# Optimization experiments

Measured on AMD Instinct MI355X. Metric: run time of the kernel, lower is better.

## Reference

```python
import jax, jax.numpy as jnp
import numpy as np

DIM = 2048
N_HEADS = 32
N_KV_HEADS = 8
HEAD_DIM = DIM // N_HEADS  # 64
GROUP = N_HEADS // N_KV_HEADS  # 4
ROPE_BASE = 10000.0


def setup_inputs() -> dict:
    key = jax.random.key(0)
    k1, k2, k3, k4, k5 = jax.random.split(key, 5)
    b, s = 1, 2048
    scale = 1.0 / np.sqrt(DIM)
    return {
        "x": jax.random.normal(k1, (b, s, DIM), dtype=jnp.float32),
        # weights stored as (in, out); equivalent math to torch Linear (x @ W.T)
        "wq": jax.random.normal(k2, (DIM, N_HEADS * HEAD_DIM), dtype=jnp.float32) * scale,
        "wk": jax.random.normal(k3, (DIM, N_KV_HEADS * HEAD_DIM), dtype=jnp.float32) * scale,
        "wv": jax.random.normal(k4, (DIM, N_KV_HEADS * HEAD_DIM), dtype=jnp.float32) * scale,
        "wo": jax.random.normal(k5, (N_HEADS * HEAD_DIM, DIM), dtype=jnp.float32) * scale,
    }


def _rope_cos_sin(seq_len, dtype):
    inv_freq = 1.0 / (ROPE_BASE ** (jnp.arange(0, HEAD_DIM, 2, dtype=jnp.float32) / HEAD_DIM))
    t = jnp.arange(seq_len, dtype=jnp.float32)
    freqs = jnp.outer(t, inv_freq)              # [s, hd/2]
    emb = jnp.concatenate([freqs, freqs], -1)   # [s, hd]
    return jnp.cos(emb).astype(dtype), jnp.sin(emb).astype(dtype)


def _rotate_half(x):
    x1, x2 = x[..., : HEAD_DIM // 2], x[..., HEAD_DIM // 2 :]
    return jnp.concatenate([-x2, x1], axis=-1)


def reference(x, wq, wk, wv, wo):
    b, s, _ = x.shape
    q = (x @ wq).reshape(b, s, N_HEADS, HEAD_DIM)
    k = (x @ wk).reshape(b, s, N_KV_HEADS, HEAD_DIM)
    v = (x @ wv).reshape(b, s, N_KV_HEADS, HEAD_DIM)

    cos, sin = _rope_cos_sin(s, x.dtype)
    cos = cos[None, :, None, :]  # [1, s, 1, hd] broadcast over batch & heads
    sin = sin[None, :, None, :]
    q = q * cos + _rotate_half(q) * sin
    k = k * cos + _rotate_half(k) * sin

    # GQA: repeat KV heads (repeat_interleave along head dim)
    k = jnp.repeat(k, GROUP, axis=2)  # [b, s, n_heads, hd]
    v = jnp.repeat(v, GROUP, axis=2)

    q = q.transpose(0, 2, 1, 3)  # [b, h, s, d]
    k = k.transpose(0, 2, 1, 3)
    v = v.transpose(0, 2, 1, 3)

    scores = jnp.einsum("bhqd,bhkd->bhqk", q, k) / jnp.sqrt(jnp.asarray(HEAD_DIM, x.dtype))
    attn = jax.nn.softmax(scores, axis=-1)
    out = jnp.einsum("bhqk,bhkd->bhqd", attn, v)
    out = out.transpose(0, 2, 1, 3).reshape(b, s, N_HEADS * HEAD_DIM)
    return out @ wo
```

## Files before the change

kernel.cpp:

```cpp
#include <hip/hip_runtime.h>
#include <hip/hip_bf16.h>

typedef __bf16 bf16x8 __attribute__((ext_vector_type(8)));
typedef __bf16 bf16x4 __attribute__((ext_vector_type(4)));
typedef __bf16 bf16x2 __attribute__((ext_vector_type(2)));
typedef float fx4 __attribute__((ext_vector_type(4)));
typedef float fx16 __attribute__((ext_vector_type(16)));

#define AS1 __attribute__((address_space(1)))
#define AS3 __attribute__((address_space(3)))

__global__ __launch_bounds__(256) void prep(const float4* __restrict__ X, __bf16* __restrict__ Xb,
                                            const float* __restrict__ wq, const float* __restrict__ wk,
                                            const float* __restrict__ wv, const float* __restrict__ wo,
                                            __bf16* __restrict__ WqkvT, __bf16* __restrict__ WoT) {
    const int bx = blockIdx.x;
    if (bx < 4096) {
        const int i = bx * 256 + threadIdx.x;
        const float4 v = X[i];
        bf16x4 o = { (__bf16)v.x, (__bf16)v.y, (__bf16)v.z, (__bf16)v.w };
        *(bf16x4*)(Xb + (size_t)i * 4) = o;
        return;
    }
    constexpr int K = 2048;
    __shared__ float t[64][33];
    const int tt = bx - 4096;
    const float* W; __bf16* Wt; int N, loc;
    if (tt < 2048)      { W = wq; Wt = WqkvT;                       N = 2048; loc = tt; }
    else if (tt < 2560) { W = wk; Wt = WqkvT + (size_t)2048 * 2048; N = 512;  loc = tt - 2048; }
    else if (tt < 3072) { W = wv; Wt = WqkvT + (size_t)2560 * 2048; N = 512;  loc = tt - 2560; }
    else                { W = wo; Wt = WoT;                         N = 2048; loc = tt - 3072; }
    const int k0 = (loc & 31) * 64, n0 = (loc >> 5) * 32;
    const int tx = threadIdx.x & 31, ty = threadIdx.x >> 5;
#pragma unroll
    for (int i = 0; i < 8; ++i)
        t[ty + i * 8][tx] = W[(size_t)(k0 + ty + i * 8) * N + n0 + tx];
    __syncthreads();
#pragma unroll
    for (int i = 0; i < 4; ++i) {
        const int nn = ty + i * 8;
        bf16x2 o = { (__bf16)t[tx * 2][nn], (__bf16)t[tx * 2 + 1][nn] };
        *(bf16x2*)&Wt[(size_t)(n0 + nn) * K + k0 + tx * 2] = o;
    }
}

__global__ __launch_bounds__(256) void gemm_qkv(const __bf16* __restrict__ A, const __bf16* __restrict__ Bt,
                                                __bf16* __restrict__ Qr, __bf16* __restrict__ Kr,
                                                __bf16* __restrict__ Vt) {
    constexpr int K = 2048;
    constexpr int BUF = 192 * 32;
    __shared__ __align__(16) __bf16 sm[4][BUF];
    const int tid = threadIdx.x;
    const int wave = tid >> 6, lane = tid & 63;
    const int quad = lane >> 4, l16 = lane & 15;
    const int m0 = blockIdx.x * 128, n0 = blockIdx.y * 64;
    fx4 acc[2][4] = {};

    const int r4 = lane >> 2;
    const int c8s = ((lane & 3) ^ ((r4 >> 1) & 3)) * 8;
    const __bf16* csrc[3]; int cdst[3];
#pragma unroll
    for (int it = 0; it < 3; ++it) {
        const int idx = wave * 3 + it;
        if (idx < 8) {
            csrc[it] = A + (size_t)(m0 + idx * 16 + r4) * K + c8s;
            cdst[it] = idx * 512 + lane * 8;
        } else {
            const int s = idx - 8;
            csrc[it] = Bt + (size_t)(n0 + s * 16 + r4) * K + c8s;
            cdst[it] = 4096 + s * 512 + lane * 8;
        }
    }
    const int colr = (quad ^ ((l16 >> 1) & 3)) * 8;
    const int arow = (wave * 32 + l16) * 32 + colr;
    const int brow = 4096 + l16 * 32 + colr;

    auto compute = [&](const __bf16* cb) {
        bf16x8 af[2], bfr[4];
#pragma unroll
        for (int i = 0; i < 2; ++i) af[i] = *(const bf16x8*)&cb[arow + i * 512];
#pragma unroll
        for (int j = 0; j < 4; ++j) bfr[j] = *(const bf16x8*)&cb[brow + j * 512];
#pragma unroll
        for (int i = 0; i < 2; ++i)
#pragma unroll
            for (int j = 0; j < 4; ++j)
                acc[i][j] = __builtin_amdgcn_mfma_f32_16x16x32_bf16(af[i], bfr[j], acc[i][j], 0, 0, 0);
    };

#pragma unroll
    for (int pt = 0; pt < 3; ++pt)
#pragma unroll
        for (int it = 0; it < 3; ++it)
            __builtin_amdgcn_global_load_lds((const AS1 void*)(csrc[it] + pt * 32),
                                             (AS3 void*)&sm[pt][cdst[it]], 16, 0, 0);

#pragma unroll 1
    for (int t = 0; t < 61; ++t) {
        asm volatile("s_waitcnt vmcnt(6) lgkmcnt(0)" ::: "memory");
        __builtin_amdgcn_s_barrier();
        const int kofs = (t + 3) * 32;
#pragma unroll
        for (int it = 0; it < 3; ++it)
            __builtin_amdgcn_global_load_lds((const AS1 void*)(csrc[it] + kofs),
                                             (AS3 void*)&sm[(t + 3) & 3][cdst[it]], 16, 0, 0);
        compute(sm[t & 3]);
    }
    asm volatile("s_waitcnt vmcnt(6) lgkmcnt(0)" ::: "memory"); __builtin_amdgcn_s_barrier(); compute(sm[1]);
    asm volatile("s_waitcnt vmcnt(3) lgkmcnt(0)" ::: "memory"); __builtin_amdgcn_s_barrier(); compute(sm[2]);
    asm volatile("s_waitcnt vmcnt(0) lgkmcnt(0)" ::: "memory"); __builtin_amdgcn_s_barrier(); compute(sm[3]);

    const int by = blockIdx.y;
    if (by < 40) {
        const float scale = (by < 32) ? 0.18033688011112042f : 1.0f;
        __bf16* base = (by < 32) ? (Qr + (size_t)by * 2048 * 64)
                                 : (Kr + (size_t)(by - 32) * 2048 * 64);
#pragma unroll
        for (int jj = 0; jj < 2; ++jj) {
            const int dlo = jj * 16 + l16;
            const float inv = __builtin_amdgcn_exp2f(-(float)dlo * 0.41524101186092029f);
#pragma unroll
            for (int i = 0; i < 2; ++i)
#pragma unroll
                for (int r = 0; r < 4; ++r) {
                    const int s = m0 + wave * 32 + i * 16 + quad * 4 + r;
                    float sn, cs;
                    __sincosf((float)s * inv, &sn, &cs);
                    const float lo = acc[i][jj][r], hv = acc[i][jj + 2][r];
                    base[(size_t)s * 64 + dlo]      = (__bf16)((lo * cs - hv * sn) * scale);
                    base[(size_t)s * 64 + dlo + 32] = (__bf16)((hv * cs + lo * sn) * scale);
                }
        }
    } else {
        __bf16* vb = Vt + (size_t)(by - 40) * 64 * 2048;
#pragma unroll
        for (int i = 0; i < 2; ++i)
#pragma unroll
            for (int j = 0; j < 4; ++j) {
                const int d = j * 16 + l16;
                const int s0 = m0 + wave * 32 + i * 16 + quad * 4;
                bf16x4 p;
#pragma unroll
                for (int r = 0; r < 4; ++r) p[r] = (__bf16)acc[i][j][r];
                *(bf16x4*)&vb[(size_t)d * 2048 + s0] = p;
            }
    }
}

__global__ __launch_bounds__(256) void gemm_out(const __bf16* __restrict__ A, const __bf16* __restrict__ Bt,
                                                float* __restrict__ C) {
    constexpr int K = 2048;
    constexpr int BUF = 192 * 32;
    __shared__ __align__(16) __bf16 sm[4][BUF];
    const int tid = threadIdx.x;
    const int wave = tid >> 6, lane = tid & 63;
    const int quad = lane >> 4, l16 = lane & 15;
    const int m0 = blockIdx.x * 128, n0 = blockIdx.y * 64;
    fx4 acc[2][4] = {};

    const int r4 = lane >> 2;
    const int c8s = ((lane & 3) ^ ((r4 >> 1) & 3)) * 8;
    const __bf16* csrc[3]; int cdst[3];
#pragma unroll
    for (int it = 0; it < 3; ++it) {
        const int idx = wave * 3 + it;
        if (idx < 8) {
            csrc[it] = A + (size_t)(m0 + idx * 16 + r4) * K + c8s;
            cdst[it] = idx * 512 + lane * 8;
        } else {
            const int s = idx - 8;
            csrc[it] = Bt + (size_t)(n0 + s * 16 + r4) * K + c8s;
            cdst[it] = 4096 + s * 512 + lane * 8;
        }
    }
    const int colr = (quad ^ ((l16 >> 1) & 3)) * 8;
    const int arow = (wave * 32 + l16) * 32 + colr;
    const int brow = 4096 + l16 * 32 + colr;

    auto compute = [&](const __bf16* cb) {
        bf16x8 af[2], bfr[4];
#pragma unroll
        for (int i = 0; i < 2; ++i) af[i] = *(const bf16x8*)&cb[arow + i * 512];
#pragma unroll
        for (int j = 0; j < 4; ++j) bfr[j] = *(const bf16x8*)&cb[brow + j * 512];
#pragma unroll
        for (int i = 0; i < 2; ++i)
#pragma unroll
            for (int j = 0; j < 4; ++j)
                acc[i][j] = __builtin_amdgcn_mfma_f32_16x16x32_bf16(af[i], bfr[j], acc[i][j], 0, 0, 0);
    };

#pragma unroll
    for (int pt = 0; pt < 3; ++pt)
#pragma unroll
        for (int it = 0; it < 3; ++it)
            __builtin_amdgcn_global_load_lds((const AS1 void*)(csrc[it] + pt * 32),
                                             (AS3 void*)&sm[pt][cdst[it]], 16, 0, 0);

#pragma unroll 1
    for (int t = 0; t < 61; ++t) {
        asm volatile("s_waitcnt vmcnt(6) lgkmcnt(0)" ::: "memory");
        __builtin_amdgcn_s_barrier();
        const int kofs = (t + 3) * 32;
#pragma unroll
        for (int it = 0; it < 3; ++it)
            __builtin_amdgcn_global_load_lds((const AS1 void*)(csrc[it] + kofs),
                                             (AS3 void*)&sm[(t + 3) & 3][cdst[it]], 16, 0, 0);
        compute(sm[t & 3]);
    }
    asm volatile("s_waitcnt vmcnt(6) lgkmcnt(0)" ::: "memory"); __builtin_amdgcn_s_barrier(); compute(sm[1]);
    asm volatile("s_waitcnt vmcnt(3) lgkmcnt(0)" ::: "memory"); __builtin_amdgcn_s_barrier(); compute(sm[2]);
    asm volatile("s_waitcnt vmcnt(0) lgkmcnt(0)" ::: "memory"); __builtin_amdgcn_s_barrier(); compute(sm[3]);

#pragma unroll
    for (int i = 0; i < 2; ++i)
#pragma unroll
        for (int j = 0; j < 4; ++j) {
            const int row = m0 + wave * 32 + i * 16 + quad * 4;
            const int col = n0 + j * 16 + l16;
#pragma unroll
            for (int r = 0; r < 4; ++r)
                C[(size_t)(row + r) * 2048 + col] = acc[i][j][r];
        }
}

__global__ __launch_bounds__(512, 4) void flash_attn(const __bf16* __restrict__ Qr, const __bf16* __restrict__ Kr,
                                                     const __bf16* __restrict__ Vt, __bf16* __restrict__ O) {
    constexpr int S = 2048;
    __shared__ __align__(16) __bf16 smem[2][4 * 64 * 72];
    const int qt = blockIdx.x, h = blockIdx.y, kvh = h >> 2;
    const int tid = threadIdx.x, wave = tid >> 6, lane = tid & 63;
    const int grp = wave >> 2, w4 = wave & 3;
    const int l32 = lane & 31, hi = lane >> 5;
    const int goff = grp * 2 * 4608;

    const int qrow = qt * 128 + w4 * 32 + l32;
    const __bf16* qptr = Qr + ((size_t)h * S + qrow) * 64;
    bf16x8 qf[4];
#pragma unroll
    for (int kc = 0; kc < 4; ++kc) qf[kc] = *(const bf16x8*)(qptr + kc * 16 + hi * 8);

    const __bf16* Kbase = Kr + (size_t)kvh * S * 64;
    const __bf16* Vbase = Vt + (size_t)kvh * 64 * S;

    const int gtid = tid & 255;
    const int krow = gtid >> 3;
    const int kcol = (gtid & 7) * 8;
    const int vslot = (kcol & 48) | ((kcol & 8) >> 1);

    bf16x8 kreg0 = *(const bf16x8*)(Kbase + (size_t)(grp * 64 + krow) * 64 + kcol);
    bf16x8 kreg1 = *(const bf16x8*)(Kbase + (size_t)(grp * 64 + 32 + krow) * 64 + kcol);
    bf16x8 vreg0 = *(const bf16x8*)(Vbase + (size_t)krow * S + grp * 64 + kcol);
    bf16x8 vreg1 = *(const bf16x8*)(Vbase + (size_t)(32 + krow) * S + grp * 64 + kcol);

    fx16 ov0, ov1;
#pragma unroll
    for (int i = 0; i < 16; ++i) { ov0[i] = 0.f; ov1[i] = 0.f; }
    float l_acc = 0.f;

    {
        __bf16* nK = &smem[0][goff];
        __bf16* nV = nK + 4608;
        *(bf16x8*)&nK[krow * 72 + kcol] = kreg0;
        *(bf16x8*)&nK[(32 + krow) * 72 + kcol] = kreg1;
        bf16x4 v0lo = { vreg0[0], vreg0[1], vreg0[2], vreg0[3] };
        bf16x4 v0hi = { vreg0[4], vreg0[5], vreg0[6], vreg0[7] };
        bf16x4 v1lo = { vreg1[0], vreg1[1], vreg1[2], vreg1[3] };
        bf16x4 v1hi = { vreg1[4], vreg1[5], vreg1[6], vreg1[7] };
        *(bf16x4*)&nV[krow * 72 + vslot]            = v0lo;
        *(bf16x4*)&nV[krow * 72 + vslot + 8]        = v0hi;
        *(bf16x4*)&nV[(32 + krow) * 72 + vslot]     = v1lo;
        *(bf16x4*)&nV[(32 + krow) * 72 + vslot + 8] = v1hi;
        const int kt1 = 2 + grp;
        kreg0 = *(const bf16x8*)(Kbase + (size_t)(kt1 * 64 + krow) * 64 + kcol);
        kreg1 = *(const bf16x8*)(Kbase + (size_t)(kt1 * 64 + 32 + krow) * 64 + kcol);
        vreg0 = *(const bf16x8*)(Vbase + (size_t)krow * S + kt1 * 64 + kcol);
        vreg1 = *(const bf16x8*)(Vbase + (size_t)(32 + krow) * S + kt1 * 64 + kcol);
    }
    __syncthreads();

    for (int it = 0; it < 16; ++it) {
        __bf16* lKg = &smem[it & 1][goff];
        __bf16* lVg = lKg + 4608;

        if (it + 1 < 16) {
            __bf16* nK = &smem[(it + 1) & 1][goff];
            __bf16* nV = nK + 4608;
            *(bf16x8*)&nK[krow * 72 + kcol] = kreg0;
            *(bf16x8*)&nK[(32 + krow) * 72 + kcol] = kreg1;
            bf16x4 v0lo = { vreg0[0], vreg0[1], vreg0[2], vreg0[3] };
            bf16x4 v0hi = { vreg0[4], vreg0[5], vreg0[6], vreg0[7] };
            bf16x4 v1lo = { vreg1[0], vreg1[1], vreg1[2], vreg1[3] };
            bf16x4 v1hi = { vreg1[4], vreg1[5], vreg1[6], vreg1[7] };
            *(bf16x4*)&nV[krow * 72 + vslot]            = v0lo;
            *(bf16x4*)&nV[krow * 72 + vslot + 8]        = v0hi;
            *(bf16x4*)&nV[(32 + krow) * 72 + vslot]     = v1lo;
            *(bf16x4*)&nV[(32 + krow) * 72 + vslot + 8] = v1hi;
            const int it2 = (it + 2 < 16) ? it + 2 : 15;
            const int ktn = it2 * 2 + grp;
            kreg0 = *(const bf16x8*)(Kbase + (size_t)(ktn * 64 + krow) * 64 + kcol);
            kreg1 = *(const bf16x8*)(Kbase + (size_t)(ktn * 64 + 32 + krow) * 64 + kcol);
            vreg0 = *(const bf16x8*)(Vbase + (size_t)krow * S + ktn * 64 + kcol);
            vreg1 = *(const bf16x8*)(Vbase + (size_t)(32 + krow) * S + ktn * 64 + kcol);
        }

        fx16 sc0, sc1;
#pragma unroll
        for (int i = 0; i < 16; ++i) { sc0[i] = 0.f; sc1[i] = 0.f; }
#pragma unroll
        for (int kc = 0; kc < 4; ++kc) {
            const bf16x8 a0 = *(const bf16x8*)&lKg[l32 * 72 + kc * 16 + hi * 8];
            const bf16x8 a1 = *(const bf16x8*)&lKg[(32 + l32) * 72 + kc * 16 + hi * 8];
            sc0 = __builtin_amdgcn_mfma_f32_32x32x16_bf16(a0, qf[kc], sc0, 0, 0, 0);
            sc1 = __builtin_amdgcn_mfma_f32_32x32x16_bf16(a1, qf[kc], sc1, 0, 0, 0);
        }

#pragma unroll
        for (int h2 = 0; h2 < 2; ++h2) {
#pragma unroll
            for (int c = 0; c < 2; ++c) {
                bf16x8 pb;
#pragma unroll
                for (int j = 0; j < 8; ++j) {
                    const float sv = h2 ? sc1[c * 8 + j] : sc0[c * 8 + j];
                    const float p = __builtin_amdgcn_exp2f(sv);
                    l_acc += p;
                    pb[j] = (__bf16)p;
                }
                const int kcv = h2 * 2 + c;
                const bf16x8 va0 = *(const bf16x8*)&lVg[l32 * 72 + kcv * 16 + hi * 8];
                const bf16x8 va1 = *(const bf16x8*)&lVg[(32 + l32) * 72 + kcv * 16 + hi * 8];
                ov0 = __builtin_amdgcn_mfma_f32_32x32x16_bf16(va0, pb, ov0, 0, 0, 0);
                ov1 = __builtin_amdgcn_mfma_f32_32x32x16_bf16(va1, pb, ov1, 0, 0, 0);
            }
        }
        __syncthreads();
    }

    const float l_pair = l_acc + __shfl_xor(l_acc, 32, 64);

    fx4* lO = (fx4*)&smem[0][0];
    float* lL = (float*)(&smem[0][0] + 16384);
    if (grp == 1) {
#pragma unroll
        for (int ic = 0; ic < 4; ++ic) {
            fx4 c0, c1;
#pragma unroll
            for (int r = 0; r < 4; ++r) { c0[r] = ov0[ic * 4 + r]; c1[r] = ov1[ic * 4 + r]; }
            lO[(ic * 4 + w4) * 64 + lane] = c0;
            lO[((ic + 4) * 4 + w4) * 64 + lane] = c1;
        }
        if (hi == 0) lL[w4 * 32 + l32] = l_pair;
    }
    __syncthreads();
    if (grp == 0) {
#pragma unroll
        for (int ic = 0; ic < 4; ++ic) {
            const fx4 c0 = lO[(ic * 4 + w4) * 64 + lane];
            const fx4 c1 = lO[((ic + 4) * 4 + w4) * 64 + lane];
#pragma unroll
            for (int r = 0; r < 4; ++r) { ov0[ic * 4 + r] += c0[r]; ov1[ic * 4 + r] += c1[r]; }
        }
        const float inv_l = 1.0f / (l_pair + lL[w4 * 32 + l32]);
#pragma unroll
        for (int dt = 0; dt < 2; ++dt)
#pragma unroll
            for (int rg2 = 0; rg2 < 4; ++rg2) {
                bf16x4 o4;
#pragma unroll
                for (int r = 0; r < 4; ++r)
                    o4[r] = (__bf16)((dt ? ov1[rg2 * 4 + r] : ov0[rg2 * 4 + r]) * inv_l);
                const int col = h * 64 + dt * 32 + rg2 * 8 + hi * 4;
                *(bf16x4*)(O + (size_t)qrow * 2048 + col) = o4;
            }
    }
}

extern "C" void kernel_launch(void* const* d_in, const int* in_sizes, int n_in,
                              void* d_out, int out_size, void* d_ws, size_t ws_size,
                              hipStream_t stream) {
    const float* x  = (const float*)d_in[0];
    const float* wq = (const float*)d_in[1];
    const float* wk = (const float*)d_in[2];
    const float* wv = (const float*)d_in[3];
    const float* wo = (const float*)d_in[4];
    float* out = (float*)d_out;
    char* ws = (char*)d_ws;

    __bf16* Xb    = (__bf16*)ws;
    __bf16* WqkvT = (__bf16*)(ws + ((size_t)8 << 20));
    __bf16* WoT   = (__bf16*)(ws + ((size_t)20 << 20));
    __bf16* Qr    = (__bf16*)(ws + ((size_t)28 << 20));
    __bf16* Kr    = (__bf16*)(ws + ((size_t)36 << 20));
    __bf16* Vt    = (__bf16*)(ws + ((size_t)38 << 20));
    __bf16* Ob    = (__bf16*)(ws + ((size_t)40 << 20));

    prep<<<4096 + 5120, 256, 0, stream>>>((const float4*)x, Xb, wq, wk, wv, wo, WqkvT, WoT);
    gemm_qkv<<<dim3(16, 48), 256, 0, stream>>>(Xb, WqkvT, Qr, Kr, Vt);
    flash_attn<<<dim3(16, 32), 512, 0, stream>>>(Qr, Kr, Vt, Ob);
    gemm_out<<<dim3(16, 32), 256, 0, stream>>>(Ob, WoT, out);
}
```

Measured before the change: 215.4 us.

## Enlarge GEMM tiles to 128x128 with 2x2 wave grid, block swizzle and MFMA priority hints

Both projection GEMMs move from 128x64 block tiles to 128x128 tiles, with each wave computing a 64x64 sub-tile (4x4 MFMAs) and the shared code pulled into a macro. A 1D grid with a block-index swizzle groups blocks that share operand tiles, and the K loop is unrolled by four with sched barriers. s_setprio is raised around MFMA bursts in the GEMMs and in flash attention, where __syncthreads is also replaced by an explicit waitcnt plus barrier. The larger tiles cut global and LDS traffic per FLOP but halve the block count (384 and 256 blocks) and raise register and LDS use, which may hurt occupancy and wave balance.

```diff
diff --git a/kernel.cpp b/kernel.cpp
--- a/kernel.cpp
+++ b/kernel.cpp
@@ -44,86 +44,102 @@
     }
 }
 
-__global__ __launch_bounds__(256) void gemm_qkv(const __bf16* __restrict__ A, const __bf16* __restrict__ Bt,
-                                                __bf16* __restrict__ Qr, __bf16* __restrict__ Kr,
-                                                __bf16* __restrict__ Vt) {
-    constexpr int K = 2048;
-    constexpr int BUF = 192 * 32;
-    __shared__ __align__(16) __bf16 sm[4][BUF];
-    const int tid = threadIdx.x;
-    const int wave = tid >> 6, lane = tid & 63;
-    const int quad = lane >> 4, l16 = lane & 15;
-    const int m0 = blockIdx.x * 128, n0 = blockIdx.y * 64;
-    fx4 acc[2][4] = {};
-
-    const int r4 = lane >> 2;
-    const int c8s = ((lane & 3) ^ ((r4 >> 1) & 3)) * 8;
-    const __bf16* csrc[3]; int cdst[3];
-#pragma unroll
-    for (int it = 0; it < 3; ++it) {
-        const int idx = wave * 3 + it;
-        if (idx < 8) {
-            csrc[it] = A + (size_t)(m0 + idx * 16 + r4) * K + c8s;
-            cdst[it] = idx * 512 + lane * 8;
-        } else {
-            const int s = idx - 8;
-            csrc[it] = Bt + (size_t)(n0 + s * 16 + r4) * K + c8s;
-            cdst[it] = 4096 + s * 512 + lane * 8;
-        }
-    }
-    const int colr = (quad ^ ((l16 >> 1) & 3)) * 8;
-    const int arow = (wave * 32 + l16) * 32 + colr;
-    const int brow = 4096 + l16 * 32 + colr;
-
-    auto compute = [&](const __bf16* cb) {
-        bf16x8 af[2], bfr[4];
-#pragma unroll
-        for (int i = 0; i < 2; ++i) af[i] = *(const bf16x8*)&cb[arow + i * 512];
-#pragma unroll
-        for (int j = 0; j < 4; ++j) bfr[j] = *(const bf16x8*)&cb[brow + j * 512];
-#pragma unroll
-        for (int i = 0; i < 2; ++i)
-#pragma unroll
-            for (int j = 0; j < 4; ++j)
-                acc[i][j] = __builtin_amdgcn_mfma_f32_16x16x32_bf16(af[i], bfr[j], acc[i][j], 0, 0, 0);
-    };
-
-#pragma unroll
-    for (int pt = 0; pt < 3; ++pt)
-#pragma unroll
-        for (int it = 0; it < 3; ++it)
-            __builtin_amdgcn_global_load_lds((const AS1 void*)(csrc[it] + pt * 32),
-                                             (AS3 void*)&sm[pt][cdst[it]], 16, 0, 0);
-
-#pragma unroll 1
-    for (int t = 0; t < 61; ++t) {
-        asm volatile("s_waitcnt vmcnt(6) lgkmcnt(0)" ::: "memory");
-        __builtin_amdgcn_s_barrier();
-        const int kofs = (t + 3) * 32;
-#pragma unroll
-        for (int it = 0; it < 3; ++it)
-            __builtin_amdgcn_global_load_lds((const AS1 void*)(csrc[it] + kofs),
-                                             (AS3 void*)&sm[(t + 3) & 3][cdst[it]], 16, 0, 0);
-        compute(sm[t & 3]);
-    }
-    asm volatile("s_waitcnt vmcnt(6) lgkmcnt(0)" ::: "memory"); __builtin_amdgcn_s_barrier(); compute(sm[1]);
-    asm volatile("s_waitcnt vmcnt(3) lgkmcnt(0)" ::: "memory"); __builtin_amdgcn_s_barrier(); compute(sm[2]);
-    asm volatile("s_waitcnt vmcnt(0) lgkmcnt(0)" ::: "memory"); __builtin_amdgcn_s_barrier(); compute(sm[3]);
-
-    const int by = blockIdx.y;
-    if (by < 40) {
-        const float scale = (by < 32) ? 0.18033688011112042f : 1.0f;
-        __bf16* base = (by < 32) ? (Qr + (size_t)by * 2048 * 64)
-                                 : (Kr + (size_t)(by - 32) * 2048 * 64);
+#define GEMM_SETUP(Aptr, Btptr)                                                              \
+    constexpr int K = 2048;                                                                  \
+    __shared__ __align__(16) __bf16 sm[4][8192];                                  \
+    const int tid = threadIdx.x;                                                             \
+    const int wave = tid >> 6, lane = tid & 63;                                              \
+    const int quad = lane >> 4, l16 = lane & 15;                                             \
+    const int wm = (wave >> 1) * 64, wn = (wave & 1) * 64;                                   \
+    fx4 acc[4][4] = {};                                                                      \
+    const int r4 = lane >> 2;                                                                \
+    const int c8s = ((lane & 3) ^ ((r4 >> 1) & 3)) * 8;                                      \
+    const __bf16* csrc[4]; int cdst[4];                                                      \
+    _Pragma("unroll")                                                                        \
+    for (int it = 0; it < 4; ++it) {                                                         \
+        const int idx = wave * 4 + it;                                                       \
+        if (idx < 8) { csrc[it] = (Aptr) + (size_t)(m0 + idx * 16 + r4) * K + c8s;           \
+                       cdst[it] = idx * 512 + lane * 8; }                                    \
+        else         { csrc[it] = (Btptr) + (size_t)(n0 + (idx - 8) * 16 + r4) * K + c8s;    \
+                       cdst[it] = 4096 + (idx - 8) * 512 + lane * 8; }                       \
+    }                                                                                        \
+    const int colr = (quad ^ ((l16 >> 1) & 3)) * 8;                                          \
+    const int arow = (wm + l16) * 32 + colr;                                                 \
+    const int brow = 4096 + (wn + l16) * 32 + colr;                                          \
+    auto compute = [&](const __bf16* cb) {                                                   \
+        bf16x8 af[4], bfr[4];                                                                \
+        _Pragma("unroll") for (int i = 0; i < 4; ++i) af[i]  = *(const bf16x8*)&cb[arow + i * 512]; \
+        _Pragma("unroll") for (int j = 0; j < 4; ++j) bfr[j] = *(const bf16x8*)&cb[brow + j * 512]; \
+        __builtin_amdgcn_s_setprio(1);                                                       \
+        _Pragma("unroll") for (int i = 0; i < 4; ++i)                                        \
+            _Pragma("unroll") for (int j = 0; j < 4; ++j)                                    \
+                acc[i][j] = __builtin_amdgcn_mfma_f32_16x16x32_bf16(af[i], bfr[j], acc[i][j], 0, 0, 0); \
+        __builtin_amdgcn_s_setprio(0);                                                       \
+    };                                                                                       \
+    _Pragma("unroll")                                                                        \
+    for (int pt = 0; pt < 3; ++pt)                                                           \
+        _Pragma("unroll")                                                                    \
+        for (int it = 0; it < 4; ++it)                                                       \
+            __builtin_amdgcn_global_load_lds((const AS1 void*)(csrc[it] + pt * 32),          \
+                                             (AS3 void*)&sm[pt][cdst[it]], 16, 0, 0);        \
+    _Pragma("unroll 1")                                                                      \
+    for (int tq = 0; tq < 15; ++tq) {                                                        \
+        const int t0 = tq * 4;                                                               \
+        _Pragma("unroll")                                                                    \
+        for (int u = 0; u < 4; ++u) {                                                        \
+            asm volatile("s_waitcnt vmcnt(8) lgkmcnt(0)" ::: "memory");                      \
+            __builtin_amdgcn_s_barrier();                                                    \
+            __builtin_amdgcn_sched_barrier(0);                                               \
+            const int tile = t0 + u + 3;                                                     \
+            const int kofs = tile * 32;                                                      \
+            _Pragma("unroll")                                                                \
+            for (int it = 0; it < 4; ++it)                                                   \
+                __builtin_amdgcn_global_load_lds((const AS1 void*)(csrc[it] + kofs),         \
+                                                 (AS3 void*)&sm[(u + 3) & 3][cdst[it]], 16, 0, 0); \
+            compute(sm[u]);                                                                  \
+        }                                                                                    \
+    }                                                                                        \
+    {                            \
+        asm volatile("s_waitcnt vmcnt(8) lgkmcnt(0)" ::: "memory");                          \
+        __builtin_amdgcn_s_barrier();                                                        \
+        __builtin_amdgcn_sched_barrier(0);                                                   \
+        _Pragma("unroll")                                                                    \
+        for (int it = 0; it < 4; ++it)                                                       \
+            __builtin_amdgcn_global_load_lds((const AS1 void*)(csrc[it] + 63 * 32),          \
+                                             (AS3 void*)&sm[3][cdst[it]], 16, 0, 0);         \
+        compute(sm[0]);                                                                      \
+    }                                                                                        \
+    asm volatile("s_waitcnt vmcnt(8) lgkmcnt(0)" ::: "memory"); __builtin_amdgcn_s_barrier();\
+    __builtin_amdgcn_sched_barrier(0); compute(sm[1]);                                       \
+    asm volatile("s_waitcnt vmcnt(4) lgkmcnt(0)" ::: "memory"); __builtin_amdgcn_s_barrier();\
+    __builtin_amdgcn_sched_barrier(0); compute(sm[2]);                                       \
+    asm volatile("s_waitcnt vmcnt(0) lgkmcnt(0)" ::: "memory"); __builtin_amdgcn_s_barrier();\
+    __builtin_amdgcn_sched_barrier(0); compute(sm[3]);
+
+__global__ __launch_bounds__(256, 2) void gemm_qkv(const __bf16* __restrict__ A, const __bf16* __restrict__ Bt,
+                                                   __bf16* __restrict__ Qr, __bf16* __restrict__ Kr,
+                                                   __bf16* __restrict__ Vt) {
+    const int bid = blockIdx.x;
+    const int swz = (bid & 7) * 48 + (bid >> 3);
+    const int m0 = (swz & 15) * 128, n0 = (swz >> 4) * 128;
+
+    GEMM_SETUP(A, Bt)
+
+    const int col64 = n0 + wn;
+    if (col64 < 2560) {
+        const bool isQ = col64 < 2048;
+        const float scale = isQ ? 0.18033688011112042f : 1.0f;
+        __bf16* base = isQ ? (Qr + (size_t)(col64 >> 6) * 2048 * 64)
+                           : (Kr + (size_t)((col64 - 2048) >> 6) * 2048 * 64);
 #pragma unroll
         for (int jj = 0; jj < 2; ++jj) {
             const int dlo = jj * 16 + l16;
             const float inv = __builtin_amdgcn_exp2f(-(float)dlo * 0.41524101186092029f);
 #pragma unroll
-            for (int i = 0; i < 2; ++i)
+            for (int i = 0; i < 4; ++i)
 #pragma unroll
                 for (int r = 0; r < 4; ++r) {
-                    const int s = m0 + wave * 32 + i * 16 + quad * 4 + r;
+                    const int s = m0 + wm + i * 16 + quad * 4 + r;
                     float sn, cs;
                     __sincosf((float)s * inv, &sn, &cs);
                     const float lo = acc[i][jj][r], hv = acc[i][jj + 2][r];
@@ -132,13 +148,13 @@
                 }
         }
     } else {
-        __bf16* vb = Vt + (size_t)(by - 40) * 64 * 2048;
-#pragma unroll
-        for (int i = 0; i < 2; ++i)
+        __bf16* vb = Vt + (size_t)((col64 - 2560) >> 6) * 64 * 2048;
+#pragma unroll
+        for (int i = 0; i < 4; ++i)
 #pragma unroll
             for (int j = 0; j < 4; ++j) {
                 const int d = j * 16 + l16;
-                const int s0 = m0 + wave * 32 + i * 16 + quad * 4;
+                const int s0 = m0 + wm + i * 16 + quad * 4;
                 bf16x4 p;
 #pragma unroll
                 for (int r = 0; r < 4; ++r) p[r] = (__bf16)acc[i][j][r];
@@ -147,77 +163,20 @@
     }
 }
 
-__global__ __launch_bounds__(256) void gemm_out(const __bf16* __restrict__ A, const __bf16* __restrict__ Bt,
-                                                float* __restrict__ C) {
-    constexpr int K = 2048;
-    constexpr int BUF = 192 * 32;
-    __shared__ __align__(16) __bf16 sm[4][BUF];
-    const int tid = threadIdx.x;
-    const int wave = tid >> 6, lane = tid & 63;
-    const int quad = lane >> 4, l16 = lane & 15;
-    const int m0 = blockIdx.x * 128, n0 = blockIdx.y * 64;
-    fx4 acc[2][4] = {};
-
-    const int r4 = lane >> 2;
-    const int c8s = ((lane & 3) ^ ((r4 >> 1) & 3)) * 8;
-    const __bf16* csrc[3]; int cdst[3];
-#pragma unroll
-    for (int it = 0; it < 3; ++it) {
-        const int idx = wave * 3 + it;
-        if (idx < 8) {
-            csrc[it] = A + (size_t)(m0 + idx * 16 + r4) * K + c8s;
-            cdst[it] = idx * 512 + lane * 8;
-        } else {
-            const int s = idx - 8;
-            csrc[it] = Bt + (size_t)(n0 + s * 16 + r4) * K + c8s;
-            cdst[it] = 4096 + s * 512 + lane * 8;
-        }
-    }
-    const int colr = (quad ^ ((l16 >> 1) & 3)) * 8;
-    const int arow = (wave * 32 + l16) * 32 + colr;
-    const int brow = 4096 + l16 * 32 + colr;
-
-    auto compute = [&](const __bf16* cb) {
-        bf16x8 af[2], bfr[4];
-#pragma unroll
-        for (int i = 0; i < 2; ++i) af[i] = *(const bf16x8*)&cb[arow + i * 512];
-#pragma unroll
-        for (int j = 0; j < 4; ++j) bfr[j] = *(const bf16x8*)&cb[brow + j * 512];
-#pragma unroll
-        for (int i = 0; i < 2; ++i)
-#pragma unroll
-            for (int j = 0; j < 4; ++j)
-                acc[i][j] = __builtin_amdgcn_mfma_f32_16x16x32_bf16(af[i], bfr[j], acc[i][j], 0, 0, 0);
-    };
-
-#pragma unroll
-    for (int pt = 0; pt < 3; ++pt)
-#pragma unroll
-        for (int it = 0; it < 3; ++it)
-            __builtin_amdgcn_global_load_lds((const AS1 void*)(csrc[it] + pt * 32),
-                                             (AS3 void*)&sm[pt][cdst[it]], 16, 0, 0);
-
-#pragma unroll 1
-    for (int t = 0; t < 61; ++t) {
-        asm volatile("s_waitcnt vmcnt(6) lgkmcnt(0)" ::: "memory");
-        __builtin_amdgcn_s_barrier();
-        const int kofs = (t + 3) * 32;
-#pragma unroll
-        for (int it = 0; it < 3; ++it)
-            __builtin_amdgcn_global_load_lds((const AS1 void*)(csrc[it] + kofs),
-                                             (AS3 void*)&sm[(t + 3) & 3][cdst[it]], 16, 0, 0);
-        compute(sm[t & 3]);
-    }
-    asm volatile("s_waitcnt vmcnt(6) lgkmcnt(0)" ::: "memory"); __builtin_amdgcn_s_barrier(); compute(sm[1]);
-    asm volatile("s_waitcnt vmcnt(3) lgkmcnt(0)" ::: "memory"); __builtin_amdgcn_s_barrier(); compute(sm[2]);
-    asm volatile("s_waitcnt vmcnt(0) lgkmcnt(0)" ::: "memory"); __builtin_amdgcn_s_barrier(); compute(sm[3]);
-
-#pragma unroll
-    for (int i = 0; i < 2; ++i)
+__global__ __launch_bounds__(256, 2) void gemm_out(const __bf16* __restrict__ A, const __bf16* __restrict__ Bt,
+                                                   float* __restrict__ C) {
+    const int bid = blockIdx.x;
+    const int swz = (bid & 7) * 32 + (bid >> 3);
+    const int m0 = (swz & 15) * 128, n0 = (swz >> 4) * 128;
+
+    GEMM_SETUP(A, Bt)
+
+#pragma unroll
+    for (int i = 0; i < 4; ++i)
 #pragma unroll
         for (int j = 0; j < 4; ++j) {
-            const int row = m0 + wave * 32 + i * 16 + quad * 4;
-            const int col = n0 + j * 16 + l16;
+            const int row = m0 + wm + i * 16 + quad * 4;
+            const int col = n0 + wn + j * 16 + l16;
 #pragma unroll
             for (int r = 0; r < 4; ++r)
                 C[(size_t)(row + r) * 2048 + col] = acc[i][j][r];
@@ -277,7 +236,9 @@
         vreg0 = *(const bf16x8*)(Vbase + (size_t)krow * S + kt1 * 64 + kcol);
         vreg1 = *(const bf16x8*)(Vbase + (size_t)(32 + krow) * S + kt1 * 64 + kcol);
     }
-    __syncthreads();
+    asm volatile("s_waitcnt lgkmcnt(0)" ::: "memory");
+    __builtin_amdgcn_s_barrier();
+    __builtin_amdgcn_sched_barrier(0);
 
     for (int it = 0; it < 16; ++it) {
         __bf16* lKg = &smem[it & 1][goff];
@@ -307,6 +268,7 @@
         fx16 sc0, sc1;
 #pragma unroll
         for (int i = 0; i < 16; ++i) { sc0[i] = 0.f; sc1[i] = 0.f; }
+        __builtin_amdgcn_s_setprio(1);
 #pragma unroll
         for (int kc = 0; kc < 4; ++kc) {
             const bf16x8 a0 = *(const bf16x8*)&lKg[l32 * 72 + kc * 16 + hi * 8];
@@ -314,6 +276,7 @@
             sc0 = __builtin_amdgcn_mfma_f32_32x32x16_bf16(a0, qf[kc], sc0, 0, 0, 0);
             sc1 = __builtin_amdgcn_mfma_f32_32x32x16_bf16(a1, qf[kc], sc1, 0, 0, 0);
         }
+        __builtin_amdgcn_s_setprio(0);
 
 #pragma unroll
         for (int h2 = 0; h2 < 2; ++h2) {
@@ -330,11 +293,15 @@
                 const int kcv = h2 * 2 + c;
                 const bf16x8 va0 = *(const bf16x8*)&lVg[l32 * 72 + kcv * 16 + hi * 8];
                 const bf16x8 va1 = *(const bf16x8*)&lVg[(32 + l32) * 72 + kcv * 16 + hi * 8];
+                __builtin_amdgcn_s_setprio(1);
                 ov0 = __builtin_amdgcn_mfma_f32_32x32x16_bf16(va0, pb, ov0, 0, 0, 0);
                 ov1 = __builtin_amdgcn_mfma_f32_32x32x16_bf16(va1, pb, ov1, 0, 0, 0);
+                __builtin_amdgcn_s_setprio(0);
             }
         }
-        __syncthreads();
+        asm volatile("s_waitcnt lgkmcnt(0)" ::: "memory");
+        __builtin_amdgcn_s_barrier();
+        __builtin_amdgcn_sched_barrier(0);
     }
 
     const float l_pair = l_acc + __shfl_xor(l_acc, 32, 64);
@@ -396,7 +363,7 @@
     __bf16* Ob    = (__bf16*)(ws + ((size_t)40 << 20));
 
     prep<<<4096 + 5120, 256, 0, stream>>>((const float4*)x, Xb, wq, wk, wv, wo, WqkvT, WoT);
-    gemm_qkv<<<dim3(16, 48), 256, 0, stream>>>(Xb, WqkvT, Qr, Kr, Vt);
+    gemm_qkv<<<384, 256, 0, stream>>>(Xb, WqkvT, Qr, Kr, Vt);
     flash_attn<<<dim3(16, 32), 512, 0, stream>>>(Qr, Kr, Vt, Ob);
-    gemm_out<<<dim3(16, 32), 256, 0, stream>>>(Ob, WoT, out);
-}
+    gemm_out<<<256, 256, 0, stream>>>(Ob, WoT, out);
+}
```

After: 199.8 us. 1.08x faster.
